# Optimization experiments

Measured on AMD Instinct MI355X. Metric: run time of the kernel, lower is better.

## Reference

```python
import jax, jax.numpy as jnp
import numpy as np

HEADS = 4
DIM_HEAD = 32
SCALE = 10.0
EPS = 1e-12  # F.normalize eps


def setup_inputs() -> dict:
    key = jax.random.key(0)
    k0, k1, k2 = jax.random.split(key, 3)
    b, c, h, w = 4, 256, 64, 64
    hidden = HEADS * DIM_HEAD  # 128
    x = jax.random.normal(k0, (b, c, h, w), dtype=jnp.float32)
    # 1x1 convs == per-pixel linear layers; store as [out_ch, in_ch]
    w_qkv = jax.random.normal(k1, (3 * hidden, c), dtype=jnp.float32) * (1.0 / np.sqrt(c))
    w_out = jax.random.normal(k2, (c, hidden), dtype=jnp.float32) * (1.0 / np.sqrt(hidden))
    b_out = jnp.zeros((c,), dtype=jnp.float32)
    return {"x": x, "w_qkv": w_qkv, "w_out": w_out, "b_out": b_out}


def _l2norm(t):
    # normalize along the per-head feature dim d (axis=2 of [b,h,d,n])
    n = jnp.sqrt(jnp.sum(t * t, axis=2, keepdims=True))
    return t / jnp.maximum(n, EPS)


def reference(x, w_qkv, w_out, b_out):
    b, c, h, w = x.shape
    n = h * w
    # to_qkv 1x1 conv (no bias)
    qkv = jnp.einsum('oc,bchw->bohw', w_qkv, x)          # [b, 3*hidden, h, w]
    qkv = qkv.reshape(b, 3, HEADS, DIM_HEAD, n)          # chunk dim=1 then split heads
    q, k, v = qkv[:, 0], qkv[:, 1], qkv[:, 2]            # each [b, heads, d, n]
    q = _l2norm(q)
    k = _l2norm(k)
    sim = jnp.einsum('bhdi,bhdj->bhij', q, k) * SCALE    # [b, heads, n, n]
    attn = jax.nn.softmax(sim, axis=-1)
    out = jnp.einsum('bhij,bhdj->bhid', attn, v)         # [b, heads, n, d]
    # 'b h (x y) d -> b (h d) x y'
    out = out.transpose(0, 1, 3, 2).reshape(b, HEADS * DIM_HEAD, h, w)
    # to_out 1x1 conv with bias
    return jnp.einsum('oc,bchw->bohw', w_out, out) + b_out[None, :, None, None]
```

## Files before the change

kernel.cpp:

```cpp
#include <hip/hip_runtime.h>
#include <math.h>

#define BB 4
#define CC 256
#define NHEAD 4
#define DH 32
#define NN 4096
#define HID 128

typedef _Float16 f16;
typedef _Float16 f16x8 __attribute__((ext_vector_type(8)));
typedef _Float16 f16x4 __attribute__((ext_vector_type(4)));
typedef float f32x4 __attribute__((ext_vector_type(4)));
typedef unsigned int u32x4 __attribute__((ext_vector_type(4)));

#define QPRESCALE 14.42695041f
#define NSHIFT 14.42695041f

#if __has_builtin(__builtin_amdgcn_exp2f)
#define EXP2F(x) __builtin_amdgcn_exp2f(x)
#else
#define EXP2F(x) __expf((x)*0.6931471805599453f)
#endif

__device__ __forceinline__ f16x8 cvt8(const float* p) {
    float4 a = *(const float4*)p;
    float4 b = *(const float4*)(p + 4);
    f16x8 r;
    r[0] = (f16)a.x; r[1] = (f16)a.y; r[2] = (f16)a.z; r[3] = (f16)a.w;
    r[4] = (f16)b.x; r[5] = (f16)b.y; r[6] = (f16)b.z; r[7] = (f16)b.w;
    return r;
}

#define XROW 40

__global__ __launch_bounds__(256, 4) void qkv_mega(const float* __restrict__ x,
                                                   const float* __restrict__ wq,
                                                   f16* __restrict__ qh,
                                                   f16* __restrict__ kh,
                                                   f16* __restrict__ vh) {
    __shared__ __align__(16) f16 xl[32 * XROW];
    int t = threadIdx.x;
    int wave = t >> 6, lane = t & 63;
    int quad = lane >> 4, col = lane & 15;
    int b = blockIdx.z;
    int i0 = blockIdx.x * 32;
    int o0w = blockIdx.y * 128 + wave * 32;

    int sc = t >> 3;
    int iseg = t & 7;
    const float* xb = x + (size_t)b * CC * NN + i0 + iseg * 4;

    f32x4 c[2][2];
#pragma unroll
    for (int mt = 0; mt < 2; mt++)
#pragma unroll
        for (int nt = 0; nt < 2; nt++) c[mt][nt] = f32x4{0.f, 0.f, 0.f, 0.f};

#pragma unroll
    for (int k0 = 0; k0 < CC; k0 += 32) {
        float4 xv = *(const float4*)(xb + (size_t)(k0 + sc) * NN);
        __syncthreads();
        xl[(iseg * 4 + 0) * XROW + sc] = (f16)xv.x;
        xl[(iseg * 4 + 1) * XROW + sc] = (f16)xv.y;
        xl[(iseg * 4 + 2) * XROW + sc] = (f16)xv.z;
        xl[(iseg * 4 + 3) * XROW + sc] = (f16)xv.w;
        __syncthreads();
        f16x8 bf0 = *(const f16x8*)(xl + (size_t)col * XROW + quad * 8);
        f16x8 bf1 = *(const f16x8*)(xl + (size_t)(16 + col) * XROW + quad * 8);
#pragma unroll
        for (int mt = 0; mt < 2; mt++) {
            f16x8 a = cvt8(wq + (size_t)(o0w + mt * 16 + col) * CC + k0 + quad * 8);
            c[mt][0] = __builtin_amdgcn_mfma_f32_16x16x32_f16(a, bf0, c[mt][0], 0, 0, 0);
            c[mt][1] = __builtin_amdgcn_mfma_f32_16x16x32_f16(a, bf1, c[mt][1], 0, 0, 0);
        }
    }

    if (blockIdx.y < 2) {
        int isQ = (blockIdx.y == 0);
        f16* dst = isQ ? qh : kh;
        int h = wave;
        float pre = isQ ? QPRESCALE : 1.0f;
#pragma unroll
        for (int nt = 0; nt < 2; nt++) {
            float ss = 0.f;
#pragma unroll
            for (int m2 = 0; m2 < 2; m2++)
#pragma unroll
                for (int r = 0; r < 4; r++) {
                    float v = c[m2][nt][r];
                    ss = fmaf(v, v, ss);
                }
            ss += __shfl_xor(ss, 16);
            ss += __shfl_xor(ss, 32);
            float inv = pre / fmaxf(sqrtf(ss), 1e-12f);
            size_t row = ((size_t)(b * 4 + h) * NN + i0 + nt * 16 + col) * 32;
#pragma unroll
            for (int m2 = 0; m2 < 2; m2++) {
                f16x4 st;
#pragma unroll
                for (int r = 0; r < 4; r++) st[r] = (f16)(c[m2][nt][r] * inv);
                *(f16x4*)(dst + row + m2 * 16 + quad * 4) = st;
            }
        }
    } else {
        int h = wave;
#pragma unroll
        for (int nt = 0; nt < 2; nt++) {
            int i = i0 + nt * 16 + col;
#pragma unroll
            for (int m2 = 0; m2 < 2; m2++)
#pragma unroll
                for (int r = 0; r < 4; r++)
                    vh[((size_t)(b * 4 + h) * 32 + m2 * 16 + quad * 4 + r) * NN + i] =
                        (f16)c[m2][nt][r];
        }
    }
}

#define KROW 40
#define VROW 72

__device__ __forceinline__ f16x8 expblk2(f32x4 sa, f32x4 sb) {
    u32x4 w;
    w[0] = __builtin_bit_cast(unsigned int,
            __builtin_amdgcn_cvt_pkrtz(EXP2F(sa[0]), EXP2F(sa[1])));
    w[1] = __builtin_bit_cast(unsigned int,
            __builtin_amdgcn_cvt_pkrtz(EXP2F(sa[2]), EXP2F(sa[3])));
    w[2] = __builtin_bit_cast(unsigned int,
            __builtin_amdgcn_cvt_pkrtz(EXP2F(sb[0]), EXP2F(sb[1])));
    w[3] = __builtin_bit_cast(unsigned int,
            __builtin_amdgcn_cvt_pkrtz(EXP2F(sb[2]), EXP2F(sb[3])));
    return __builtin_bit_cast(f16x8, w);
}

__device__ __forceinline__ void compute_g(const f16* kl, const f16* vl, int jb,
                                          int col, int quad, const f16x8 (&qB)[4],
                                          f32x4 (&o)[4][2], f32x4 (&lf)[4]) {
    f16x8 kA = *(const f16x8*)(kl + (jb + col) * KROW + quad * 8);
    f16x8 kB = *(const f16x8*)(kl + (jb + 16 + col) * KROW + quad * 8);
    f16x8 v0 = *(const f16x8*)(vl + col * VROW + jb + quad * 8);
    f16x8 v1 = *(const f16x8*)(vl + (16 + col) * VROW + jb + quad * 8);
    const f32x4 zs = {-NSHIFT, -NSHIFT, -NSHIFT, -NSHIFT};
    f16 one = (f16)1.0f;
    f16x8 ones = {one, one, one, one, one, one, one, one};
#pragma unroll
    for (int f = 0; f < 4; f++) {
        f32x4 sa = __builtin_amdgcn_mfma_f32_16x16x32_f16(kA, qB[f], zs, 0, 0, 0);
        f32x4 sb = __builtin_amdgcn_mfma_f32_16x16x32_f16(kB, qB[f], zs, 0, 0, 0);
        f16x8 p = expblk2(sa, sb);
        o[f][0] = __builtin_amdgcn_mfma_f32_16x16x32_f16(p, v0, o[f][0], 0, 0, 0);
        o[f][1] = __builtin_amdgcn_mfma_f32_16x16x32_f16(p, v1, o[f][1], 0, 0, 0);
        lf[f]   = __builtin_amdgcn_mfma_f32_16x16x32_f16(p, ones, lf[f], 0, 0, 0);
    }
}

template <int SPLIT>
__global__ __launch_bounds__(256, 4) void attn_mfma(const f16* __restrict__ qh,
                                                    const f16* __restrict__ kh,
                                                    const f16* __restrict__ vh,
                                                    float* __restrict__ op,
                                                    float* __restrict__ lp,
                                                    f16* __restrict__ att16) {
    __shared__ __align__(16) f16 klds[2][64 * KROW];
    __shared__ __align__(16) f16 vlds[2][32 * VROW];
    int t = threadIdx.x;
    int wave = t >> 6, lane = t & 63;
    int quad = lane >> 4, col = lane & 15;

    int bid = blockIdx.x;
    int xcd = bid & 7;
    int slot = bid >> 3;
    int bh = xcd * 2 + slot / (16 * SPLIT);
    int rem = slot % (16 * SPLIT);
    int s = rem >> 4;
    int i0 = (rem & 15) * 256;
    int iw = i0 + wave * 64;

    const int NT = 64 / SPLIT;
    int kbase = s * (NN / SPLIT);

    const f16* qb = qh + (size_t)bh * NN * 32;
    const f16* kb = kh + (size_t)bh * NN * 32 + (size_t)kbase * 32;
    const f16* vb = vh + (size_t)bh * 32 * NN + kbase;

    f16x8 qB[4];
#pragma unroll
    for (int f = 0; f < 4; f++)
        qB[f] = *(const f16x8*)(qb + (size_t)(iw + f * 16 + col) * 32 + quad * 8);

    f32x4 o[4][2], lf[4];
#pragma unroll
    for (int f = 0; f < 4; f++) {
        o[f][0] = f32x4{0.f, 0.f, 0.f, 0.f};
        o[f][1] = f32x4{0.f, 0.f, 0.f, 0.f};
        lf[f]   = f32x4{0.f, 0.f, 0.f, 0.f};
    }

    int ktr = t >> 2, kts = t & 3;
    int ksrc = (ktr & 32) | ((ktr & 12) << 1) | ((ktr & 16) >> 2) | (ktr & 3);
    int vtr = t >> 3, vts = t & 7;

    f16x8 kr, vr;
    kr = *(const f16x8*)(kb + (size_t)(0 + ksrc) * 32 + kts * 8);
    vr = *(const f16x8*)(vb + (size_t)vtr * NN + 0 + vts * 8);
    *(f16x8*)(&klds[0][0] + ktr * KROW + kts * 8) = kr;
    *(f16x8*)(&vlds[0][0] + vtr * VROW + vts * 8) = vr;
    __syncthreads();
    kr = *(const f16x8*)(kb + (size_t)(64 + ksrc) * 32 + kts * 8);
    vr = *(const f16x8*)(vb + (size_t)vtr * NN + 64 + vts * 8);

    for (int tile = 0; tile < NT - 2; tile++) {
        int buf = tile & 1;
        const f16* kl = &klds[buf][0];
        const f16* vl = &vlds[buf][0];
        compute_g(kl, vl, 0, col, quad, qB, o, lf);
        compute_g(kl, vl, 32, col, quad, qB, o, lf);
        *(f16x8*)(&klds[buf ^ 1][0] + ktr * KROW + kts * 8) = kr;
        *(f16x8*)(&vlds[buf ^ 1][0] + vtr * VROW + vts * 8) = vr;
        __syncthreads();
        int j0 = (tile + 2) * 64;
        kr = *(const f16x8*)(kb + (size_t)(j0 + ksrc) * 32 + kts * 8);
        vr = *(const f16x8*)(vb + (size_t)vtr * NN + j0 + vts * 8);
    }
    {
        compute_g(&klds[0][0], &vlds[0][0], 0, col, quad, qB, o, lf);
        compute_g(&klds[0][0], &vlds[0][0], 32, col, quad, qB, o, lf);
        *(f16x8*)(&klds[1][0] + ktr * KROW + kts * 8) = kr;
        *(f16x8*)(&vlds[1][0] + vtr * VROW + vts * 8) = vr;
        __syncthreads();
    }
    {
        compute_g(&klds[1][0], &vlds[1][0], 0, col, quad, qB, o, lf);
        compute_g(&klds[1][0], &vlds[1][0], 32, col, quad, qB, o, lf);
    }

    if constexpr (SPLIT == 1) {
        int b = bh >> 2, h = bh & 3;
        f16* ab = att16 + (size_t)b * NN * HID + h * 32;
#pragma unroll
        for (int f = 0; f < 4; f++)
#pragma unroll
            for (int r = 0; r < 4; r++) {
                float inv = __builtin_amdgcn_rcpf(lf[f][r]);
                size_t row = (size_t)(iw + f * 16 + quad * 4 + r) * HID;
                ab[row + col]      = (f16)(o[f][0][r] * inv);
                ab[row + 16 + col] = (f16)(o[f][1][r] * inv);
            }
    } else {
        float* ob = op + (size_t)(s * 16 + bh) * NN * 32;
#pragma unroll
        for (int f = 0; f < 4; f++)
#pragma unroll
            for (int r = 0; r < 4; r++) {
                size_t rr = (size_t)(iw + f * 16 + quad * 4 + r) * 32;
                ob[rr + col]      = o[f][0][r];
                ob[rr + 16 + col] = o[f][1][r];
            }
        if (col == 0) {
            float* lb = lp + (size_t)(s * 16 + bh) * NN;
#pragma unroll
            for (int f = 0; f < 4; f++)
#pragma unroll
                for (int r = 0; r < 4; r++)
                    lb[iw + f * 16 + quad * 4 + r] = lf[f][r];
        }
    }
}

#define WROW 136

template <int NS>
__global__ __launch_bounds__(256) void out_fused(const float* __restrict__ op,
                                                 const float* __restrict__ lp,
                                                 const float* __restrict__ wo,
                                                 const float* __restrict__ bo,
                                                 float* __restrict__ out) {
    __shared__ __align__(16) f16 wol[128 * WROW];
    int t = threadIdx.x;
    int wave = t >> 6, lane = t & 63;
    int quad = lane >> 4, col = lane & 15;
    int b = blockIdx.z;
    int i0w = blockIdx.x * 64 + wave * 16;
    int o0 = blockIdx.y * 128;

    {
        int row = t >> 1;
        int kh = (t & 1) * 64;
        const float* src = wo + (size_t)(o0 + row) * HID + kh;
        f16* d = wol + row * WROW + kh;
#pragma unroll
        for (int j = 0; j < 8; j++) {
            float4 a = *(const float4*)(src + j * 8);
            float4 bq = *(const float4*)(src + j * 8 + 4);
            f16x8 s;
            s[0] = (f16)a.x; s[1] = (f16)a.y; s[2] = (f16)a.z; s[3] = (f16)a.w;
            s[4] = (f16)bq.x; s[5] = (f16)bq.y; s[6] = (f16)bq.z; s[7] = (f16)bq.w;
            *(f16x8*)(d + j * 8) = s;
        }
    }
    __syncthreads();

    int i = i0w + col;
    float invl[4];
#pragma unroll
    for (int h = 0; h < 4; h++) {
        float l = 0.f;
#pragma unroll
        for (int s = 0; s < NS; s++)
            l += lp[(size_t)(s * 16 + b * 4 + h) * NN + i];
        invl[h] = __builtin_amdgcn_rcpf(l);
    }

    const f32x4 z = {0.f, 0.f, 0.f, 0.f};
    f32x4 c[8];
#pragma unroll
    for (int ot = 0; ot < 8; ot++) c[ot] = z;

#pragma unroll
    for (int k0 = 0; k0 < HID; k0 += 32) {
        int h = k0 >> 5;
        f32x4 accA = z, accB = z;
#pragma unroll
        for (int s = 0; s < NS; s++) {
            const float* src = op + ((size_t)(s * 16 + b * 4 + h) * NN + i) * 32 + quad * 8;
            accA += *(const f32x4*)(src);
            accB += *(const f32x4*)(src + 4);
        }
        float iv = invl[h];
        f16x8 a0;
        a0[0] = (f16)(accA[0] * iv); a0[1] = (f16)(accA[1] * iv);
        a0[2] = (f16)(accA[2] * iv); a0[3] = (f16)(accA[3] * iv);
        a0[4] = (f16)(accB[0] * iv); a0[5] = (f16)(accB[1] * iv);
        a0[6] = (f16)(accB[2] * iv); a0[7] = (f16)(accB[3] * iv);
#pragma unroll
        for (int ot = 0; ot < 8; ot++) {
            f16x8 bf = *(const f16x8*)(wol + (size_t)(ot * 16 + col) * WROW + k0 + quad * 8);
            c[ot] = __builtin_amdgcn_mfma_f32_16x16x32_f16(a0, bf, c[ot], 0, 0, 0);
        }
    }

#pragma unroll
    for (int ot = 0; ot < 8; ot++) {
        int o = o0 + ot * 16 + col;
        float bias = bo[o];
        int ii = i0w + quad * 4;
        float4 st = {c[ot][0] + bias, c[ot][1] + bias,
                     c[ot][2] + bias, c[ot][3] + bias};
        *(float4*)(out + ((size_t)b * CC + o) * NN + ii) = st;
    }
}

__global__ __launch_bounds__(256, 4) void out_mfma(const f16* __restrict__ att16,
                                                   const float* __restrict__ wo,
                                                   const float* __restrict__ bo,
                                                   float* __restrict__ out) {
    __shared__ __align__(16) f16 wol[64 * WROW];
    int t = threadIdx.x;
    int wave = t >> 6, lane = t & 63;
    int quad = lane >> 4, col = lane & 15;
    int b = blockIdx.z;
    int i0w = blockIdx.x * 64 + wave * 16;
    int o0 = blockIdx.y * 64;
    const f16* ab = att16 + (size_t)b * NN * HID;

    {
        int row = t >> 2;
        int kq = (t & 3) * 32;
        const float* src = wo + (size_t)(o0 + row) * HID + kq;
        f16* d = wol + row * WROW + kq;
#pragma unroll
        for (int j = 0; j < 4; j++) {
            float4 a = *(const float4*)(src + j * 8);
            float4 bq = *(const float4*)(src + j * 8 + 4);
            f16x8 s;
            s[0] = (f16)a.x; s[1] = (f16)a.y; s[2] = (f16)a.z; s[3] = (f16)a.w;
            s[4] = (f16)bq.x; s[5] = (f16)bq.y; s[6] = (f16)bq.z; s[7] = (f16)bq.w;
            *(f16x8*)(d + j * 8) = s;
        }
    }
    __syncthreads();

    const f32x4 z = {0.f, 0.f, 0.f, 0.f};
    f32x4 c[4];
#pragma unroll
    for (int ot = 0; ot < 4; ot++) c[ot] = z;

#pragma unroll
    for (int k0 = 0; k0 < HID; k0 += 32) {
        f16x8 a0 = *(const f16x8*)(ab + (size_t)(i0w + col) * HID + k0 + quad * 8);
#pragma unroll
        for (int ot = 0; ot < 4; ot++) {
            f16x8 bf = *(const f16x8*)(wol + (size_t)(ot * 16 + col) * WROW + k0 + quad * 8);
            c[ot] = __builtin_amdgcn_mfma_f32_16x16x32_f16(a0, bf, c[ot], 0, 0, 0);
        }
    }

#pragma unroll
    for (int ot = 0; ot < 4; ot++) {
        int o = o0 + ot * 16 + col;
        float bias = bo[o];
        int i = i0w + quad * 4;
        float4 st = {c[ot][0] + bias, c[ot][1] + bias,
                     c[ot][2] + bias, c[ot][3] + bias};
        *(float4*)(out + ((size_t)b * CC + o) * NN + i) = st;
    }
}

extern "C" void kernel_launch(void* const* d_in, const int* in_sizes, int n_in,
                              void* d_out, int out_size, void* d_ws, size_t ws_size,
                              hipStream_t stream) {
    const float* x     = (const float*)d_in[0];
    const float* w_qkv = (const float*)d_in[1];
    const float* w_out = (const float*)d_in[2];
    const float* b_out = (const float*)d_in[3];
    float* out = (float*)d_out;

    char* ws = (char*)d_ws;
    f16* qh    = (f16*)(ws);
    f16* kh    = (f16*)(ws + (4u << 20));
    f16* vh    = (f16*)(ws + (8u << 20));
    f16* att16 = (f16*)(ws + (12u << 20));

    qkv_mega<<<dim3(NN / 32, 3, BB), 256, 0, stream>>>(x, w_qkv, qh, kh, vh);

    if (ws_size >= (50ull << 20)) {
        float* op = (float*)(ws + (16ull << 20));
        float* lp = (float*)(ws + (48ull << 20));
        attn_mfma<4><<<dim3(1024), 256, 0, stream>>>(qh, kh, vh, op, lp, att16);
        out_fused<4><<<dim3(NN / 64, 2, BB), 256, 0, stream>>>(op, lp, w_out, b_out, out);
    } else if (ws_size >= (33ull << 20)) {
        float* op = (float*)(ws + (16ull << 20));
        float* lp = (float*)(ws + (32ull << 20));
        attn_mfma<2><<<dim3(512), 256, 0, stream>>>(qh, kh, vh, op, lp, att16);
        out_fused<2><<<dim3(NN / 64, 2, BB), 256, 0, stream>>>(op, lp, w_out, b_out, out);
    } else {
        attn_mfma<1><<<dim3(256), 256, 0, stream>>>(qh, kh, vh, nullptr, nullptr, att16);
        out_mfma<<<dim3(NN / 64, CC / 64, BB), 256, 0, stream>>>(att16, w_out, b_out, out);
    }
}
```

Measured before the change: 152.0 us.

## Load K/V fragments directly from global memory, dropping LDS staging

Removes the double-buffered LDS staging of K and V tiles and the per-tile __syncthreads. Each wave now loads its MFMA K and V fragments straight from global memory through the L2/L1 caches, with the K row permutation folded into the pointer arithmetic. This cuts LDS traffic and block-wide barriers, and may let the compiler schedule loads freely. The cost is that all four waves in a block fetch the same K/V data redundantly from cache, and latency hiding now depends on unroll-by-2 and occupancy instead of explicit prefetch.

Result: slower. 162.0 us (+6.5%).

```diff
diff --git a/kernel.cpp b/kernel.cpp
--- a/kernel.cpp
+++ b/kernel.cpp
@@ -118,9 +118,6 @@
     }
 }
 
-#define KROW 40
-#define VROW 72
-
 __device__ __forceinline__ f16x8 expblk2(f32x4 sa, f32x4 sb) {
     u32x4 w;
     w[0] = __builtin_bit_cast(unsigned int,
@@ -134,27 +131,6 @@
     return __builtin_bit_cast(f16x8, w);
 }
 
-__device__ __forceinline__ void compute_g(const f16* kl, const f16* vl, int jb,
-                                          int col, int quad, const f16x8 (&qB)[4],
-                                          f32x4 (&o)[4][2], f32x4 (&lf)[4]) {
-    f16x8 kA = *(const f16x8*)(kl + (jb + col) * KROW + quad * 8);
-    f16x8 kB = *(const f16x8*)(kl + (jb + 16 + col) * KROW + quad * 8);
-    f16x8 v0 = *(const f16x8*)(vl + col * VROW + jb + quad * 8);
-    f16x8 v1 = *(const f16x8*)(vl + (16 + col) * VROW + jb + quad * 8);
-    const f32x4 zs = {-NSHIFT, -NSHIFT, -NSHIFT, -NSHIFT};
-    f16 one = (f16)1.0f;
-    f16x8 ones = {one, one, one, one, one, one, one, one};
-#pragma unroll
-    for (int f = 0; f < 4; f++) {
-        f32x4 sa = __builtin_amdgcn_mfma_f32_16x16x32_f16(kA, qB[f], zs, 0, 0, 0);
-        f32x4 sb = __builtin_amdgcn_mfma_f32_16x16x32_f16(kB, qB[f], zs, 0, 0, 0);
-        f16x8 p = expblk2(sa, sb);
-        o[f][0] = __builtin_amdgcn_mfma_f32_16x16x32_f16(p, v0, o[f][0], 0, 0, 0);
-        o[f][1] = __builtin_amdgcn_mfma_f32_16x16x32_f16(p, v1, o[f][1], 0, 0, 0);
-        lf[f]   = __builtin_amdgcn_mfma_f32_16x16x32_f16(p, ones, lf[f], 0, 0, 0);
-    }
-}
-
 template <int SPLIT>
 __global__ __launch_bounds__(256, 4) void attn_mfma(const f16* __restrict__ qh,
                                                     const f16* __restrict__ kh,
@@ -162,8 +138,6 @@
                                                     float* __restrict__ op,
                                                     float* __restrict__ lp,
                                                     f16* __restrict__ att16) {
-    __shared__ __align__(16) f16 klds[2][64 * KROW];
-    __shared__ __align__(16) f16 vlds[2][32 * VROW];
     int t = threadIdx.x;
     int wave = t >> 6, lane = t & 63;
     int quad = lane >> 4, col = lane & 15;
@@ -177,8 +151,8 @@
     int i0 = (rem & 15) * 256;
     int iw = i0 + wave * 64;
 
-    const int NT = 64 / SPLIT;
-    int kbase = s * (NN / SPLIT);
+    const int NK = NN / SPLIT;
+    int kbase = s * NK;
 
     const f16* qb = qh + (size_t)bh * NN * 32;
     const f16* kb = kh + (size_t)bh * NN * 32 + (size_t)kbase * 32;
@@ -197,42 +171,33 @@
         lf[f]   = f32x4{0.f, 0.f, 0.f, 0.f};
     }
 
-    int ktr = t >> 2, kts = t & 3;
-    int ksrc = (ktr & 32) | ((ktr & 12) << 1) | ((ktr & 16) >> 2) | (ktr & 3);
-    int vtr = t >> 3, vts = t & 7;
-
-    f16x8 kr, vr;
-    kr = *(const f16x8*)(kb + (size_t)(0 + ksrc) * 32 + kts * 8);
-    vr = *(const f16x8*)(vb + (size_t)vtr * NN + 0 + vts * 8);
-    *(f16x8*)(&klds[0][0] + ktr * KROW + kts * 8) = kr;
-    *(f16x8*)(&vlds[0][0] + vtr * VROW + vts * 8) = vr;
-    __syncthreads();
-    kr = *(const f16x8*)(kb + (size_t)(64 + ksrc) * 32 + kts * 8);
-    vr = *(const f16x8*)(vb + (size_t)vtr * NN + 64 + vts * 8);
-
-    for (int tile = 0; tile < NT - 2; tile++) {
-        int buf = tile & 1;
-        const f16* kl = &klds[buf][0];
-        const f16* vl = &vlds[buf][0];
-        compute_g(kl, vl, 0, col, quad, qB, o, lf);
-        compute_g(kl, vl, 32, col, quad, qB, o, lf);
-        *(f16x8*)(&klds[buf ^ 1][0] + ktr * KROW + kts * 8) = kr;
-        *(f16x8*)(&vlds[buf ^ 1][0] + vtr * VROW + vts * 8) = vr;
-        __syncthreads();
-        int j0 = (tile + 2) * 64;
-        kr = *(const f16x8*)(kb + (size_t)(j0 + ksrc) * 32 + kts * 8);
-        vr = *(const f16x8*)(vb + (size_t)vtr * NN + j0 + vts * 8);
-    }
-    {
-        compute_g(&klds[0][0], &vlds[0][0], 0, col, quad, qB, o, lf);
-        compute_g(&klds[0][0], &vlds[0][0], 32, col, quad, qB, o, lf);
-        *(f16x8*)(&klds[1][0] + ktr * KROW + kts * 8) = kr;
-        *(f16x8*)(&vlds[1][0] + vtr * VROW + vts * 8) = vr;
-        __syncthreads();
-    }
-    {
-        compute_g(&klds[1][0], &vlds[1][0], 0, col, quad, qB, o, lf);
-        compute_g(&klds[1][0], &vlds[1][0], 32, col, quad, qB, o, lf);
+    int rA = col, rB = 16 + col;
+    int pA = ((rA & 12) << 1) | ((rA & 16) >> 2) | (rA & 3);
+    int pB = ((rB & 12) << 1) | ((rB & 16) >> 2) | (rB & 3);
+    const f16* kAp = kb + (size_t)pA * 32 + quad * 8;
+    const f16* kBp = kb + (size_t)pB * 32 + quad * 8;
+    const f16* v0p = vb + (size_t)col * NN + quad * 8;
+    const f16* v1p = vb + (size_t)(16 + col) * NN + quad * 8;
+
+    const f32x4 zs = {-NSHIFT, -NSHIFT, -NSHIFT, -NSHIFT};
+    f16 one = (f16)1.0f;
+    f16x8 ones = {one, one, one, one, one, one, one, one};
+
+#pragma unroll 2
+    for (int j = 0; j < NK; j += 32) {
+        f16x8 kA = *(const f16x8*)(kAp + (size_t)j * 32);
+        f16x8 kB = *(const f16x8*)(kBp + (size_t)j * 32);
+        f16x8 v0 = *(const f16x8*)(v0p + j);
+        f16x8 v1 = *(const f16x8*)(v1p + j);
+#pragma unroll
+        for (int f = 0; f < 4; f++) {
+            f32x4 sa = __builtin_amdgcn_mfma_f32_16x16x32_f16(kA, qB[f], zs, 0, 0, 0);
+            f32x4 sb = __builtin_amdgcn_mfma_f32_16x16x32_f16(kB, qB[f], zs, 0, 0, 0);
+            f16x8 p = expblk2(sa, sb);
+            o[f][0] = __builtin_amdgcn_mfma_f32_16x16x32_f16(p, v0, o[f][0], 0, 0, 0);
+            o[f][1] = __builtin_amdgcn_mfma_f32_16x16x32_f16(p, v1, o[f][1], 0, 0, 0);
+            lf[f]   = __builtin_amdgcn_mfma_f32_16x16x32_f16(p, ones, lf[f], 0, 0, 0);
+        }
     }
 
     if constexpr (SPLIT == 1) {
```
